# Kernel tuning notes

Measured on AMD Instinct MI355X. Metric: run time of the kernel, lower is better.

Reference implementation:

```python
import jax, jax.numpy as jnp
import numpy as np
from jax import lax

B, Q, H, W = 2, 2304, 64, 64
ENC_OUT = 64          # encoder out_dim
DIM = 192             # base_dim
HEAD = 8
R = 3
RA = (2 * R + 1) ** 2  # 49 local-window positions
CF = 64                # pe enc_dims // 2 (complex channels)
ENC_DIMS = 2 * CF      # 128
IN_DIM = (DIM + ENC_DIMS) * RA + 2  # 15682
HID = 256


def conv3(x, w, b):
    y = lax.conv_general_dilated(x, w, (1, 1), 'SAME',
                                 dimension_numbers=('NCHW', 'OIHW', 'NCHW'))
    return y + b[None, :, None, None]


def _flat_gather(img, idx):
    # img [B,C,HW], idx [B,...] -> [B,C,...]
    return jax.vmap(lambda f, i: f[:, i])(img, idx)


def gather_nearest(img, c):
    # grid_sample nearest, align_corners=False, zeros padding. c [B,Q,K,2] (y,x)
    Bc, C, Hc, Wc = img.shape
    py = ((c[..., 0] + 1) * Hc - 1) / 2
    px = ((c[..., 1] + 1) * Wc - 1) / 2
    iy = jnp.round(py); ix = jnp.round(px)
    valid = (iy >= 0) & (iy < Hc) & (ix >= 0) & (ix < Wc)
    idx = (jnp.clip(iy, 0, Hc - 1) * Wc + jnp.clip(ix, 0, Wc - 1)).astype(jnp.int32)
    g = _flat_gather(img.reshape(Bc, C, Hc * Wc), idx)  # [B,C,Q,K]
    g = jnp.where(valid[:, None], g, 0.0)
    return g.transpose(0, 2, 3, 1)  # [B,Q,K,C]


def gather_bilinear_zeros(img, c):
    # grid_sample bilinear, align_corners=False, zeros padding. c [B,Q,K,2]
    Bc, C, Hc, Wc = img.shape
    py = ((c[..., 0] + 1) * Hc - 1) / 2
    px = ((c[..., 1] + 1) * Wc - 1) / 2
    y0f = jnp.floor(py); x0f = jnp.floor(px)
    wy = py - y0f; wx = px - x0f
    y0 = y0f.astype(jnp.int32); x0 = x0f.astype(jnp.int32)
    flat = img.reshape(Bc, C, Hc * Wc)
    def corner(yi, xi, w):
        valid = (yi >= 0) & (yi < Hc) & (xi >= 0) & (xi < Wc)
        idx = jnp.clip(yi, 0, Hc - 1) * Wc + jnp.clip(xi, 0, Wc - 1)
        return _flat_gather(flat, idx) * (w * valid)[:, None]
    out = (corner(y0, x0, (1 - wy) * (1 - wx)) + corner(y0, x0 + 1, (1 - wy) * wx)
           + corner(y0 + 1, x0, wy * (1 - wx)) + corner(y0 + 1, x0 + 1, wy * wx))
    return out.transpose(0, 2, 3, 1)


def gather_bilinear_border(img, c):
    # grid_sample bilinear, align_corners=False, border padding. c [B,Q,2]
    Bc, C, Hc, Wc = img.shape
    py = jnp.clip(((c[..., 0] + 1) * Hc - 1) / 2, 0, Hc - 1)
    px = jnp.clip(((c[..., 1] + 1) * Wc - 1) / 2, 0, Wc - 1)
    y0f = jnp.floor(py); x0f = jnp.floor(px)
    wy = py - y0f; wx = px - x0f
    y0 = y0f.astype(jnp.int32); x0 = x0f.astype(jnp.int32)
    y1 = jnp.minimum(y0 + 1, Hc - 1); x1 = jnp.minimum(x0 + 1, Wc - 1)
    flat = img.reshape(Bc, C, Hc * Wc)
    g = lambda yi, xi: _flat_gather(flat, yi * Wc + xi)  # [B,C,Q]
    out = (g(y0, x0) * ((1 - wy) * (1 - wx))[:, None]
           + g(y0, x1) * ((1 - wy) * wx)[:, None]
           + g(y1, x0) * (wy * (1 - wx))[:, None]
           + g(y1, x1) * (wy * wx)[:, None])
    return out.transpose(0, 2, 1)  # [B,Q,C]


def _forward(inp, coord, cell, enc_w, enc_b, qw, qb, kw, kb, vw, vb, fw, fb,
             pbw, pbb, pew, w1, b1, w2, b2):
    feat = conv3(inp, enc_w, enc_b)            # encoder (simplified)
    fq = conv3(feat, qw, qb); fk = conv3(feat, kw, kb)
    fv = conv3(feat, vw, vb); ff = conv3(feat, fw, fb)
    Bq, Qn = coord.shape[:2]
    Hf, Wf = feat.shape[-2:]
    dk = DIM // HEAD
    c = jnp.clip(coord, -1 + 1e-6, 1 - 1e-6)[:, :, None, :]   # [B,Q,1,2]
    # nearest feature-grid pixel-center coordinates (= grid_sample nearest of coord_lr)
    iy = jnp.round(((c[..., 0] + 1) * Hf - 1) / 2)
    ix = jnp.round(((c[..., 1] + 1) * Wf - 1) / 2)
    ck0 = jnp.stack([-1 + (2 * iy + 1) / Hf, -1 + (2 * ix + 1) / Wf], axis=-1)
    dh = jnp.linspace(-R, R, 2 * R + 1) * 2 / Hf
    dw = jnp.linspace(-R, R, 2 * R + 1) * 2 / Wf
    delta = jnp.stack(jnp.meshgrid(dh, dw, indexing='ij'), axis=-1).reshape(1, 1, RA, 2)
    ck = ck0 + delta                                          # [B,Q,49,2]
    q_ = gather_bilinear_zeros(fq, c)[:, :, 0].reshape(Bq, Qn, HEAD, dk)
    k_ = gather_nearest(fk, ck).reshape(Bq, Qn, RA, HEAD, dk)
    v_ = gather_nearest(fv, ck).reshape(Bq, Qn, RA, HEAD, dk)
    fr = gather_nearest(ff, ck)                               # [B,Q,49,CF]
    hw = jnp.array([Hf, Wf], dtype=coord.dtype)
    rel = (coord[:, :, None, :] - ck) * hw                    # [B,Q,49,2]
    rel_cell = cell * hw
    sim = jnp.einsum('bqhd,bqkhd->bqkh', q_, k_) / np.sqrt(dk).astype(np.float32)
    pb = rel @ pbw + pbb                                      # positional bias [B,Q,49,HEAD]
    attn = jax.nn.softmax(sim + pb, axis=2)                   # softmax over the 49 window slots
    attn_map = attn[0, 10, :, 0].reshape(2 * R + 1, 2 * R + 1, 1)
    v_weighted = (v_ * attn[..., None]).reshape(Bq, Qn, RA, DIM)
    frc = jnp.fft.fft2(fr.reshape(Bq, Qn, 2 * R + 1, 2 * R + 1, CF),
                       axes=(2, 3), norm='ortho').reshape(Bq, Qn, RA, CF)
    phase = rel @ pew                                         # Fourier PE: exp(i*phase)
    enc = lax.complex(jnp.cos(phase), jnp.sin(phase)) * frc
    enc = jnp.stack([enc.real, enc.imag], axis=-1).reshape(Bq, Qn, RA, ENC_DIMS)
    out = jnp.concatenate([v_weighted, enc], axis=-1).reshape(Bq, Qn, -1)
    out = jnp.concatenate([out, rel_cell], axis=-1)           # [B,Q,IN_DIM]
    pred = jax.nn.relu(out @ w1 + b1) @ w2 + b2               # imnet MLP
    ret = pred + gather_bilinear_border(inp, coord)           # global residual
    return ret, attn_map


def setup_inputs() -> dict:
    key = jax.random.key(0)
    ks = jax.random.split(key, 20)
    def n(k, shape, s=0.05):
        return jax.random.normal(k, shape, dtype=jnp.float32) * s
    inp = jax.random.normal(ks[0], (B, 3, H, W), dtype=jnp.float32)
    coord = jax.random.uniform(ks[1], (B, Q, 2), minval=-1.0, maxval=1.0, dtype=jnp.float32)
    cell = jnp.full((B, Q, 2), 2.0 / 128, dtype=jnp.float32)
    return {
        'inp': inp, 'coord': coord, 'cell': cell,
        'enc_w': n(ks[2], (ENC_OUT, 3, 3, 3)), 'enc_b': n(ks[3], (ENC_OUT,)),
        'qw': n(ks[4], (DIM, ENC_OUT, 3, 3)), 'qb': n(ks[5], (DIM,)),
        'kw': n(ks[6], (DIM, ENC_OUT, 3, 3)), 'kb': n(ks[7], (DIM,)),
        'vw': n(ks[8], (DIM, ENC_OUT, 3, 3)), 'vb': n(ks[9], (DIM,)),
        'fw': n(ks[10], (CF, ENC_OUT, 3, 3)), 'fb': n(ks[11], (CF,)),
        'pbw': n(ks[12], (2, HEAD), 0.5), 'pbb': n(ks[13], (HEAD,), 0.5),
        'pew': n(ks[14], (2, CF), 0.5),
        'w1': n(ks[15], (IN_DIM, HID), 0.01), 'b1': n(ks[16], (HID,)),
        'w2': n(ks[17], (HID, 3), 0.05), 'b2': n(ks[18], (3,)),
    }


def reference(inp, coord, cell, enc_w, enc_b, qw, qb, kw, kb, vw, vb, fw, fb,
              pbw, pbb, pew, w1, b1, w2, b2):
    return _forward(inp, coord, cell, enc_w, enc_b, qw, qb, kw, kb, vw, vb,
                    fw, fb, pbw, pbb, pew, w1, b1, w2, b2)
```

## Files before the change

### kernel.cpp

```cpp
#include <hip/hip_runtime.h>

typedef unsigned short u16t;
typedef unsigned int   u32t;
typedef __attribute__((ext_vector_type(8))) short short8;
typedef __attribute__((ext_vector_type(4))) float f32x4;

#define B_    2
#define QN    2304
#define NQ    4608
#define HWS   64
#define ENCC  64
#define DIMC  192
#define NHEAD 8
#define DKH   24
#define RAW   49
#define CFC   64
#define FRP   68
#define CMAP  640
#define KCONV 576
#define INDIM 15682
#define KPAD  16128
#define HIDN  256
#define PIX   8192
#define SPLITK 12
#define KSLICE (KPAD/SPLITK)

__device__ __forceinline__ float b2f(u16t u){ u32t v=((u32t)u)<<16; return __builtin_bit_cast(float,v); }
__device__ __forceinline__ u16t f2b(float f){ u32t v=__builtin_bit_cast(u32t,f); return (u16t)((v + 0x7FFFu + ((v>>16)&1u))>>16); }

#define GLOAD16(SRC, DST) __builtin_amdgcn_global_load_lds( \
  (const __attribute__((address_space(1))) unsigned int*)(const void*)(SRC), \
  (__attribute__((address_space(3))) unsigned int*)(void*)(DST), 16, 0, 0)

__global__ __launch_bounds__(256) void k_enc(const float* __restrict__ inp, const float* __restrict__ ew,
                      const float* __restrict__ eb, u16t* __restrict__ feat){
  int i = blockIdx.x*256+threadIdx.x;
  if(i>=B_*HWS*HWS*ENCC) return;
  int oc=i&63, x=(i>>6)&63, y=(i>>12)&63, b=i>>18;
  float acc = eb[oc];
  for(int c=0;c<3;c++)
    for(int dy=0;dy<3;dy++){
      int yy=y+dy-1; if(yy<0||yy>=HWS) continue;
      for(int dx=0;dx<3;dx++){
        int xx=x+dx-1; if(xx<0||xx>=HWS) continue;
        acc += inp[((b*3+c)*HWS+yy)*HWS+xx] * ew[((oc*3+c)*3+dy)*3+dx];
      }
    }
  feat[i]=f2b(acc);
}

__global__ __launch_bounds__(256) void k_w1t(const float* __restrict__ w1, u16t* __restrict__ w1t){
  __shared__ u16t t[64][65];
  int kb = blockIdx.x*64, nb = blockIdx.y*64;
  for(int i=threadIdx.x;i<4096;i+=256){
    int k=i>>6, n=i&63; int gk=kb+k;
    t[k][n] = (gk<INDIM) ? f2b(w1[(size_t)gk*HIDN + nb + n]) : (u16t)0;
  }
  __syncthreads();
  for(int i=threadIdx.x;i<4096;i+=256){
    int n=i>>6, k=i&63;
    w1t[(size_t)(nb+n)*KPAD + kb + k] = t[k][n];
  }
}

__global__ __launch_bounds__(256) void k_wconv(const float* qw,const float* kw,const float* vw,const float* fw,
                        const float* qb,const float* kb_,const float* vb,const float* fb,
                        u16t* __restrict__ wct, float* __restrict__ bias){
  int i = blockIdx.x*256+threadIdx.x;
  if(i < CMAP*KCONV){
    int oc=i/KCONV, kk=i%KCONV;
    int ic=kk&63, tap=kk>>6;
    const float* w; int ol=oc;
    if(oc<192) w=qw;
    else if(oc<384){w=kw; ol=oc-192;}
    else if(oc<576){w=vw; ol=oc-384;}
    else {w=fw; ol=oc-576;}
    wct[(size_t)oc*KCONV + kk] = f2b(w[(ol*64+ic)*9 + tap]);
  }
  if(i<CMAP){
    bias[i] = (i<192)? qb[i] : (i<384? kb_[i-192] : (i<576? vb[i-384] : fb[i-576]));
  }
}

__global__ __launch_bounds__(256) void k_im2col(const u16t* __restrict__ feat, u16t* __restrict__ A){
  int i = blockIdx.x*256+threadIdx.x;
  if(i>=PIX*72) return;
  int k8=i%72, pix=i/72;
  int tap=k8/8, ic8=(k8&7)<<3;
  int x=pix&63, y=(pix>>6)&63, b=pix>>12;
  int yy=y+tap/3-1, xx=x+tap%3-1;
  uint4 v;
  if(yy>=0&&yy<HWS&&xx>=0&&xx<HWS) v = *(const uint4*)&feat[(size_t)(((b*HWS+yy)*HWS+xx)*ENCC)+ic8];
  else v = make_uint4(0u,0u,0u,0u);
  *(uint4*)&A[(size_t)pix*KCONV + tap*64 + ic8] = v;
}

__global__ __launch_bounds__(256) void k_gemm128(const u16t* __restrict__ A, int lda,
    const u16t* __restrict__ BT, int ldb, const float* __restrict__ bias,
    void* __restrict__ Cout, int ldc, int kslice, int mode){
  __shared__ __align__(16) u16t As[128*64];
  __shared__ __align__(16) u16t Bs[128*64];
  int m0 = blockIdx.x*128, n0 = blockIdx.y*128;
  int tid = threadIdx.x;
  int wave = tid>>6, lane = tid&63;
  int wm = wave>>1, wn = wave&1;
  int kg = lane>>4, l16 = lane&15;
  int kbeg = blockIdx.z*kslice, kend = kbeg+kslice;
  f32x4 acc[4][4] = {};
  for(int k0=kbeg;k0<kend;k0+=64){
    __syncthreads();
    #pragma unroll
    for(int j=0;j<4;j++){
      int seg = (wave*4+j)*64 + lane;
      int row = seg>>3, qp = seg&7;
      int q = qp ^ (row&7);
      GLOAD16(&A [(size_t)(m0+row)*lda + k0 + q*8], &As[(wave*4+j)*512]);
      GLOAD16(&BT[(size_t)(n0+row)*ldb + k0 + q*8], &Bs[(wave*4+j)*512]);
    }
    __syncthreads();
    #pragma unroll
    for(int kk=0;kk<2;kk++){
      int ks = kk*4 + kg;
      short8 a[4], b[4];
      #pragma unroll
      for(int mf=0;mf<4;mf++){
        int row = wm*64+mf*16+l16;
        a[mf] = *(const short8*)&As[row*64 + (ks^(row&7))*8];
      }
      #pragma unroll
      for(int nf=0;nf<4;nf++){
        int row = wn*64+nf*16+l16;
        b[nf] = *(const short8*)&Bs[row*64 + (ks^(row&7))*8];
      }
      #pragma unroll
      for(int mf=0;mf<4;mf++)
        #pragma unroll
        for(int nf=0;nf<4;nf++)
          acc[mf][nf] = __builtin_amdgcn_mfma_f32_16x16x32_bf16(a[mf], b[nf], acc[mf][nf], 0,0,0);
    }
  }
  int l4 = lane>>4;
  if(mode==0){
    u16t* C16 = (u16t*)Cout;
    #pragma unroll
    for(int mf=0;mf<4;mf++){
      #pragma unroll
      for(int nf=0;nf<4;nf++){
        #pragma unroll
        for(int r=0;r<4;r++){
          int gm = m0 + wm*64 + mf*16 + l4*4 + r;
          int gn = n0 + wn*64 + nf*16 + l16;
          C16[(size_t)gm*ldc+gn] = f2b(acc[mf][nf][r] + bias[gn]);
        }
      }
    }
  } else {
    u16t* C16 = (u16t*)Cout + (size_t)blockIdx.z * (size_t)(gridDim.x*128) * ldc;
    #pragma unroll
    for(int mf=0;mf<4;mf++){
      #pragma unroll
      for(int nf=0;nf<4;nf++){
        #pragma unroll
        for(int r=0;r<4;r++){
          int gm = m0 + wm*64 + mf*16 + l4*4 + r;
          int gn = n0 + wn*64 + nf*16 + l16;
          C16[(size_t)gm*ldc+gn] = f2b(acc[mf][nf][r]);
        }
      }
    }
  }
}

__global__ __launch_bounds__(256) void k_redout(const u16t* __restrict__ hidp, const float* __restrict__ b1,
                      const float* __restrict__ w2, const float* __restrict__ b2v,
                      const float* __restrict__ inp, const float* __restrict__ coord,
                      float* __restrict__ outp, int M, int q0){
  int i = blockIdx.x*256+threadIdx.x;
  if(i>=M*64) return;
  int q=i>>6, lane=i&63, n4=lane*4;
  f32x4 acc = *(const f32x4*)&b1[n4];
  for(int s=0;s<SPLITK;s++){
    uint2 t = *(const uint2*)&hidp[((size_t)s*M + q)*HIDN + n4];
    acc.x += b2f((u16t)t.x); acc.y += b2f((u16t)(t.x>>16));
    acc.z += b2f((u16t)t.y); acc.w += b2f((u16t)(t.y>>16));
  }
  float h0=fmaxf(acc.x,0.f), h1=fmaxf(acc.y,0.f), h2=fmaxf(acc.z,0.f), h3=fmaxf(acc.w,0.f);
  float p0 = h0*w2[n4*3+0] + h1*w2[(n4+1)*3+0] + h2*w2[(n4+2)*3+0] + h3*w2[(n4+3)*3+0];
  float p1 = h0*w2[n4*3+1] + h1*w2[(n4+1)*3+1] + h2*w2[(n4+2)*3+1] + h3*w2[(n4+3)*3+1];
  float p2 = h0*w2[n4*3+2] + h1*w2[(n4+1)*3+2] + h2*w2[(n4+2)*3+2] + h3*w2[(n4+3)*3+2];
  #pragma unroll
  for(int m=1;m<64;m<<=1){
    p0 += __shfl_xor(p0, m);
    p1 += __shfl_xor(p1, m);
    p2 += __shfl_xor(p2, m);
  }
  if(lane<3){
    int qg = q0 + q;
    int j = lane;
    float accj = (j==0? p0 : (j==1? p1 : p2)) + b2v[j];
    int b=qg/QN;
    float cy=coord[qg*2], cx=coord[qg*2+1];
    float py=fminf(fmaxf(((cy+1.f)*64.f-1.f)*0.5f,0.f),63.f);
    float px=fminf(fmaxf(((cx+1.f)*64.f-1.f)*0.5f,0.f),63.f);
    float y0f=floorf(py), x0f=floorf(px);
    float wy=py-y0f, wx=px-x0f;
    int y0=(int)y0f, x0=(int)x0f;
    int y1=min(y0+1,63), x1=min(x0+1,63);
    const float* ip=&inp[(size_t)(b*3+j)*4096];
    float g00=ip[y0*64+x0], g01=ip[y0*64+x1];
    float g10=ip[y1*64+x0], g11=ip[y1*64+x1];
    float res=g00*(1.f-wy)*(1.f-wx)+g01*(1.f-wy)*wx+g10*wy*(1.f-wx)+g11*wy*wx;
    outp[qg*3+j]=accj+res;
  }
}

__global__ __launch_bounds__(256) void k_feat(const float* __restrict__ coord, const float* __restrict__ cell,
                       const u16t* __restrict__ maps, const float* __restrict__ pbw,
                       const float* __restrict__ pbb, const float* __restrict__ pew,
                       u16t* __restrict__ F, float* __restrict__ outAttn, int q0){
  __shared__ float q_lds[DIMC];
  __shared__ float relsy[RAW], relsx[RAW];
  __shared__ int   wbase[RAW];
  __shared__ float sa[RAW][NHEAD];
  __shared__ float fr_lds[RAW*FRP];
  __shared__ float c7[7], s7[7];
  __shared__ float pewf0[CFC], pewf1[CFC];
  __shared__ float pbwf0[NHEAD], pbwf1[NHEAD], pbbf[NHEAD];

  int qg = q0 + blockIdx.x;
  int b  = qg / QN;
  int tid = threadIdx.x;
  float cy = coord[qg*2], cx = coord[qg*2+1];
  const float lo = -1.0f + 1e-6f, hi = 1.0f - 1e-6f;
  float ccy = fminf(fmaxf(cy,lo),hi), ccx = fminf(fmaxf(cx,lo),hi);
  float pyq = ((ccy+1.f)*64.f - 1.f)*0.5f, pxq = ((ccx+1.f)*64.f - 1.f)*0.5f;
  int iy = (int)rintf(pyq), ix = (int)rintf(pxq);

  if(tid < RAW){
    int ki = tid/7, kj = tid%7;
    int yy = iy + ki - 3, xx = ix + kj - 3;
    wbase[tid] = (yy>=0&&yy<64&&xx>=0&&xx<64) ? ((b*64+yy)*64+xx)*CMAP : -1;
    float ck_y = (-1.f + (float)(2*iy+1)*(1.f/64.f)) + (float)(ki-3)*(2.f/64.f);
    float ck_x = (-1.f + (float)(2*ix+1)*(1.f/64.f)) + (float)(kj-3)*(2.f/64.f);
    relsy[tid] = (cy - ck_y)*64.f;
    relsx[tid] = (cx - ck_x)*64.f;
  }
  if(tid<7){ float ang = -6.283185307179586f * (float)tid / 7.f; c7[tid]=cosf(ang); s7[tid]=sinf(ang); }
  if(tid<CFC){ pewf0[tid]=pew[tid]; pewf1[tid]=pew[CFC+tid]; }
  if(tid<NHEAD){ pbwf0[tid]=pbw[tid]; pbwf1[tid]=pbw[NHEAD+tid]; pbbf[tid]=pbb[tid]; }
  __syncthreads();

  if(tid < DIMC){
    float y0f=floorf(pyq), x0f=floorf(pxq);
    float wy=pyq-y0f, wx=pxq-x0f;
    int y0=(int)y0f, x0=(int)x0f;
    float acc=0.f;
    for(int ty=0;ty<2;ty++) for(int tx=0;tx<2;tx++){
      int yy=y0+ty, xx=x0+tx;
      if(yy<0||yy>=64||xx<0||xx>=64) continue;
      float w=(ty? wy:1.f-wy)*(tx? wx:1.f-wx);
      acc += w * b2f(maps[(size_t)((b*64+yy)*64+xx)*CMAP + tid]);
    }
    q_lds[tid]=acc;
  }
  for(int i=tid;i<RAW*8;i+=256){
    int k=i>>3, c8=(i&7)<<3;
    int base=wbase[k];
    f32x4 lo4={0.f,0.f,0.f,0.f}, hi4={0.f,0.f,0.f,0.f};
    if(base>=0){
      uint4 t = *(const uint4*)&maps[(size_t)base + 576 + c8];
      lo4 = f32x4{b2f((u16t)t.x), b2f((u16t)(t.x>>16)), b2f((u16t)t.y), b2f((u16t)(t.y>>16))};
      hi4 = f32x4{b2f((u16t)t.z), b2f((u16t)(t.z>>16)), b2f((u16t)t.w), b2f((u16t)(t.w>>16))};
    }
    *(f32x4*)&fr_lds[k*FRP+c8]   = lo4;
    *(f32x4*)&fr_lds[k*FRP+c8+4] = hi4;
  }
  __syncthreads();

  for(int i=tid;i<RAW*NHEAD;i+=256){
    int k=i>>3, h=i&7;
    int base=wbase[k];
    float dot=0.f;
    if(base>=0){
      const u16t* p = &maps[(size_t)base + DIMC + h*DKH];
      for(int c8=0;c8<3;c8++){
        uint4 t = *(const uint4*)&p[c8*8];
        u32t a4[4]={t.x,t.y,t.z,t.w};
        for(int j=0;j<4;j++){
          dot += q_lds[h*DKH + c8*8 + 2*j]   * b2f((u16t)a4[j]);
          dot += q_lds[h*DKH + c8*8 + 2*j+1] * b2f((u16t)(a4[j]>>16));
        }
      }
    }
    sa[k][h] = dot/sqrtf(24.f) + relsy[k]*pbwf0[h] + relsx[k]*pbwf1[h] + pbbf[h];
  }
  __syncthreads();

  if(tid < 64){
    int h = tid>>3, sub = tid&7;
    float m = -1e30f;
    for(int k=sub;k<RAW;k+=8) m = fmaxf(m, sa[k][h]);
    #pragma unroll
    for(int mm=1;mm<8;mm<<=1) m = fmaxf(m, __shfl_xor(m, mm));
    float s = 0.f;
    for(int k=sub;k<RAW;k+=8){ float e=__expf(sa[k][h]-m); sa[k][h]=e; s+=e; }
    #pragma unroll
    for(int mm=1;mm<8;mm<<=1) s += __shfl_xor(s, mm);
    float inv = 1.f/s;
    for(int k=sub;k<RAW;k+=8) sa[k][h]*=inv;
  }
  __syncthreads();
  if(qg==10 && tid<RAW) outAttn[tid] = sa[tid][0];

  size_t frow = (size_t)(qg-q0)*KPAD;
  for(int i=tid;i<RAW*24;i+=256){
    int k=i/24, c8=(i%24)*8;
    int base=wbase[k];
    u32t o[4]={0,0,0,0};
    if(base>=0){
      uint4 t = *(const uint4*)&maps[(size_t)base + 384 + c8];
      u32t a4[4]={t.x,t.y,t.z,t.w};
      for(int j=0;j<4;j++){
        int c0=c8+2*j;
        u16t r0=f2b(b2f((u16t)a4[j])      * sa[k][ c0   /DKH]);
        u16t r1=f2b(b2f((u16t)(a4[j]>>16))* sa[k][(c0+1)/DKH]);
        o[j] = (u32t)r0 | ((u32t)r1<<16);
      }
    }
    *(uint4*)&F[frow + (size_t)k*320 + c8] = make_uint4(o[0],o[1],o[2],o[3]);
  }
  for(int idx=INDIM-2+tid; idx<KPAD; idx+=256){
    u16t v=0;
    if(idx==15680) v=f2b(cell[qg*2]*64.f);
    else if(idx==15681) v=f2b(cell[qg*2+1]*64.f);
    F[frow+idx]=v;
  }

  #pragma unroll
  for(int pp=0;pp<2;pp++){
    int p = tid + pp*256;
    if(p < 448){
      int v_ = p>>6, c = p&63;
      float Gr[7], Gi[7];
      #pragma unroll
      for(int a_=0;a_<7;a_++){
        float re=0.f, im=0.f;
        #pragma unroll
        for(int bb=0;bb<7;bb++){
          float f=fr_lds[(a_*7+bb)*FRP+c];
          int m=(v_*bb)%7;
          re += f*c7[m]; im += f*s7[m];
        }
        Gr[a_]=re; Gi[a_]=im;
      }
      float pw0=pewf0[c], pw1=pewf1[c];
      #pragma unroll
      for(int u=0;u<7;u++){
        int k = u*7 + v_;
        float tr=0.f, ti=0.f;
        #pragma unroll
        for(int a_=0;a_<7;a_++){
          int m=(u*a_)%7;
          float cc=c7[m], ss=s7[m];
          tr += Gr[a_]*cc - Gi[a_]*ss;
          ti += Gr[a_]*ss + Gi[a_]*cc;
        }
        tr*=(1.f/7.f); ti*=(1.f/7.f);
        float ph = relsy[k]*pw0 + relsx[k]*pw1;
        float sp, cp; __sincosf(ph, &sp, &cp);
        float er = cp*tr - sp*ti, ei = cp*ti + sp*tr;
        u32t pk = (u32t)f2b(er) | ((u32t)f2b(ei)<<16);
        *(u32t*)&F[frow + (size_t)k*320 + 192 + 2*c] = pk;
      }
    }
  }
}

__global__ __launch_bounds__(256) void k_mark(float* __restrict__ outp, int n, float val){
  int i = blockIdx.x*256+threadIdx.x;
  if(i<n) outp[i]=val;
}

extern "C" void kernel_launch(void* const* d_in, const int* in_sizes, int n_in,
                              void* d_out, int out_size, void* d_ws, size_t ws_size,
                              hipStream_t stream){
  int I_inp, I_coord, I_cell, I_encw, I_encb, I_qw, I_qb, I_kw, I_kb, I_vw, I_vb,
      I_fw, I_fb, I_pbw, I_pbb, I_pew, I_w1, I_b1, I_w2, I_b2;
  bool dictOrder = (n_in==20 && in_sizes[0]==24576 && in_sizes[1]==9216 && in_sizes[3]==1728
                    && in_sizes[5]==110592 && in_sizes[16]==4014592 && in_sizes[19]==3);
  bool sortOrder = (n_in==20 && in_sizes[0]==256 && in_sizes[1]==3 && in_sizes[8]==24576
                    && in_sizes[10]==110592 && in_sizes[18]==4014592 && in_sizes[19]==768);
  if(dictOrder){
    I_inp=0; I_coord=1; I_cell=2; I_encw=3; I_encb=4; I_qw=5; I_qb=6; I_kw=7; I_kb=8;
    I_vw=9; I_vb=10; I_fw=11; I_fb=12; I_pbw=13; I_pbb=14; I_pew=15; I_w1=16; I_b1=17; I_w2=18; I_b2=19;
  } else if(sortOrder){
    I_b1=0; I_b2=1; I_cell=2; I_coord=3; I_encb=4; I_encw=5; I_fb=6; I_fw=7; I_inp=8;
    I_kb=9; I_kw=10; I_pbb=11; I_pbw=12; I_pew=13; I_qb=14; I_qw=15; I_vb=16; I_vw=17; I_w1=18; I_w2=19;
  } else {
    float mark = (float)(n_in==20 ? in_sizes[0] : 1000000+n_in);
    k_mark<<<dim3((out_size+255)/256), dim3(256), 0, stream>>>((float*)d_out, out_size, mark);
    return;
  }

  const float* inp  =(const float*)d_in[I_inp];
  const float* coord=(const float*)d_in[I_coord];
  const float* cell =(const float*)d_in[I_cell];
  const float* enc_w=(const float*)d_in[I_encw];
  const float* enc_b=(const float*)d_in[I_encb];
  const float* qw=(const float*)d_in[I_qw];
  const float* qb=(const float*)d_in[I_qb];
  const float* kw=(const float*)d_in[I_kw];
  const float* kbp=(const float*)d_in[I_kb];
  const float* vw=(const float*)d_in[I_vw];
  const float* vb=(const float*)d_in[I_vb];
  const float* fw=(const float*)d_in[I_fw];
  const float* fb=(const float*)d_in[I_fb];
  const float* pbw=(const float*)d_in[I_pbw];
  const float* pbb=(const float*)d_in[I_pbb];
  const float* pew=(const float*)d_in[I_pew];
  const float* w1=(const float*)d_in[I_w1];
  const float* b1=(const float*)d_in[I_b1];
  const float* w2=(const float*)d_in[I_w2];
  const float* b2v=(const float*)d_in[I_b2];
  float* outp=(float*)d_out;

  char* ws=(char*)d_ws;
  size_t off=0;
  auto alloc=[&](size_t bytes){ size_t o=off; off=(off+bytes+255)&~(size_t)255; return o; };
  size_t o_feat = alloc((size_t)PIX*ENCC*2);
  size_t o_imc  = alloc((size_t)PIX*KCONV*2);
  size_t o_wct  = alloc((size_t)CMAP*KCONV*2);
  size_t o_cb   = alloc((size_t)CMAP*4);
  size_t o_maps = alloc((size_t)PIX*CMAP*2);
  size_t o_w1t  = alloc((size_t)HIDN*KPAD*2);
  size_t fixed = off;
  size_t rem = (ws_size>fixed)? ws_size-fixed : 0;
  size_t perQ = (size_t)KPAD*2 + (size_t)SPLITK*HIDN*2;
  long long cq = (long long)(rem/perQ);
  int chunkQ = (int)((cq/128)*128);
  if(chunkQ>NQ) chunkQ=NQ;
  size_t o_F, o_hp;
  if(chunkQ>=128){
    o_F  = alloc((size_t)chunkQ*KPAD*2);
    o_hp = alloc((size_t)SPLITK*chunkQ*HIDN*2);
  } else {
    chunkQ = 128;
    o_F  = o_imc;
    o_hp = (o_imc + (size_t)128*KPAD*2 + 255) & ~(size_t)255;
  }

  u16t*  feat=(u16t*)(ws+o_feat);
  u16t*  imc =(u16t*)(ws+o_imc);
  u16t*  wct =(u16t*)(ws+o_wct);
  float* cbias=(float*)(ws+o_cb);
  u16t*  maps=(u16t*)(ws+o_maps);
  u16t*  w1t =(u16t*)(ws+o_w1t);
  u16t*  Fb  =(u16t*)(ws+o_F);
  u16t*  hidp=(u16t*)(ws+o_hp);

  k_w1t   <<<dim3(KPAD/64, HIDN/64), dim3(256), 0, stream>>>(w1, w1t);
  k_wconv <<<dim3((CMAP*KCONV+255)/256), dim3(256), 0, stream>>>(qw,kw,vw,fw,qb,kbp,vb,fb,wct,cbias);
  k_enc   <<<dim3((PIX*ENCC+255)/256), dim3(256), 0, stream>>>(inp,enc_w,enc_b,feat);
  k_im2col<<<dim3((PIX*72+255)/256), dim3(256), 0, stream>>>(feat,imc);
  k_gemm128<<<dim3(PIX/128, CMAP/128, 1), dim3(256), 0, stream>>>(imc, KCONV, wct, KCONV, cbias,
            (void*)maps, CMAP, KCONV, 0);

  for(int q0=0;q0<NQ;q0+=chunkQ){
    int nq = (NQ-q0 < chunkQ) ? (NQ-q0) : chunkQ;
    k_feat<<<dim3(nq), dim3(256), 0, stream>>>(coord,cell,maps,pbw,pbb,pew,Fb,outp+13824,q0);
    k_gemm128<<<dim3(nq/128, HIDN/128, SPLITK), dim3(256), 0, stream>>>(Fb, KPAD, w1t, KPAD, b1,
            (void*)hidp, HIDN, KSLICE, 2);
    k_redout<<<dim3((nq*64+255)/256), dim3(256), 0, stream>>>(hidp, b1, w2, b2v, inp, coord,
            outp, nq, q0);
  }
}
```

Before: 179.1 us.

## Double-buffer LDS tiles in k_gemm128 with 32-wide K steps

Restructures the GEMM main loop to use two LDS buffers with a K-tile of 32 instead of one buffer with a K-tile of 64. The next tile's global-to-LDS load is issued before the MFMAs on the current tile, and each iteration needs one barrier instead of two. The aim is to hide global load latency behind compute. In exchange, each barrier covers half as much MFMA work, and the XOR swizzle drops to 4 chunks per row, which may raise LDS bank conflicts. Correctness relies on the async loads having completed by the next barrier.

```diff
diff --git a/kernel.cpp b/kernel.cpp
--- a/kernel.cpp
+++ b/kernel.cpp
@@ -98,46 +98,48 @@
 __global__ __launch_bounds__(256) void k_gemm128(const u16t* __restrict__ A, int lda,
     const u16t* __restrict__ BT, int ldb, const float* __restrict__ bias,
     void* __restrict__ Cout, int ldc, int kslice, int mode){
-  __shared__ __align__(16) u16t As[128*64];
-  __shared__ __align__(16) u16t Bs[128*64];
+  __shared__ __align__(16) u16t As[2][128*32];
+  __shared__ __align__(16) u16t Bs[2][128*32];
   int m0 = blockIdx.x*128, n0 = blockIdx.y*128;
   int tid = threadIdx.x;
   int wave = tid>>6, lane = tid&63;
   int wm = wave>>1, wn = wave&1;
   int kg = lane>>4, l16 = lane&15;
-  int kbeg = blockIdx.z*kslice, kend = kbeg+kslice;
+  int kbeg = blockIdx.z*kslice;
+  int nt = kslice>>5;
+  auto STAGE = [&](int buf, int k0){
+    #pragma unroll
+    for(int s=0;s<2;s++){
+      int seg = (wave*2+s)*64 + lane;
+      int row = seg>>2, qp = seg&3;
+      int q = qp ^ (row&3);
+      GLOAD16(&A [(size_t)(m0+row)*lda + k0 + q*8], &As[buf][(wave*2+s)*512]);
+      GLOAD16(&BT[(size_t)(n0+row)*ldb + k0 + q*8], &Bs[buf][(wave*2+s)*512]);
+    }
+  };
   f32x4 acc[4][4] = {};
-  for(int k0=kbeg;k0<kend;k0+=64){
+  int cur = 0;
+  STAGE(0, kbeg);
+  for(int t=0;t<nt;t++){
     __syncthreads();
-    #pragma unroll
-    for(int j=0;j<4;j++){
-      int seg = (wave*4+j)*64 + lane;
-      int row = seg>>3, qp = seg&7;
-      int q = qp ^ (row&7);
-      GLOAD16(&A [(size_t)(m0+row)*lda + k0 + q*8], &As[(wave*4+j)*512]);
-      GLOAD16(&BT[(size_t)(n0+row)*ldb + k0 + q*8], &Bs[(wave*4+j)*512]);
-    }
-    __syncthreads();
-    #pragma unroll
-    for(int kk=0;kk<2;kk++){
-      int ks = kk*4 + kg;
-      short8 a[4], b[4];
+    if(t+1<nt) STAGE(cur^1, kbeg+(t+1)*32);
+    short8 a[4], b[4];
+    #pragma unroll
+    for(int mf=0;mf<4;mf++){
+      int row = wm*64+mf*16+l16;
+      a[mf] = *(const short8*)&As[cur][row*32 + (kg^(row&3))*8];
+    }
+    #pragma unroll
+    for(int nf=0;nf<4;nf++){
+      int row = wn*64+nf*16+l16;
+      b[nf] = *(const short8*)&Bs[cur][row*32 + (kg^(row&3))*8];
+    }
+    #pragma unroll
+    for(int mf=0;mf<4;mf++)
       #pragma unroll
-      for(int mf=0;mf<4;mf++){
-        int row = wm*64+mf*16+l16;
-        a[mf] = *(const short8*)&As[row*64 + (ks^(row&7))*8];
-      }
-      #pragma unroll
-      for(int nf=0;nf<4;nf++){
-        int row = wn*64+nf*16+l16;
-        b[nf] = *(const short8*)&Bs[row*64 + (ks^(row&7))*8];
-      }
-      #pragma unroll
-      for(int mf=0;mf<4;mf++)
-        #pragma unroll
-        for(int nf=0;nf<4;nf++)
-          acc[mf][nf] = __builtin_amdgcn_mfma_f32_16x16x32_bf16(a[mf], b[nf], acc[mf][nf], 0,0,0);
-    }
+      for(int nf=0;nf<4;nf++)
+        acc[mf][nf] = __builtin_amdgcn_mfma_f32_16x16x32_bf16(a[mf], b[nf], acc[mf][nf], 0,0,0);
+    cur ^= 1;
   }
   int l4 = lane>>4;
   if(mode==0){
```

Result: slower. 192.2 us (+7.3%).
